# Performance work log

Measured on AMD Instinct MI355X. Metric: run time of the kernel, lower is better.

## Reference

```python
import jax, jax.numpy as jnp
import numpy as np

K = 1024       # vq_codebook_size
DC = 64        # vq_code_dim
BETA = 0.25    # commitment cost
DECAY = 0.99   # EMA decay
EPS = 1e-05


def setup_inputs() -> dict:
    key = jax.random.key(0)
    k1, k2, k3 = jax.random.split(key, 3)
    B, H, W = 32, 64, 64
    return {
        "z_e": jax.random.normal(k1, (B, DC, H, W), dtype=jnp.float32),
        "embedding": jax.random.normal(k2, (K, DC), dtype=jnp.float32),
        "cluster_size": jnp.ones((K,), dtype=jnp.float32),
        "embed_avg": jax.random.normal(k3, (K, DC), dtype=jnp.float32),
    }


def reference(z_e, embedding, cluster_size, embed_avg):
    B, D, H, W = z_e.shape
    # flat: [N, D] detached codes, N = B*H*W
    flat = jax.lax.stop_gradient(z_e).transpose(0, 2, 3, 1).reshape(-1, D).astype(jnp.float32)
    distances = ((flat ** 2).sum(1, keepdims=True)
                 + (embedding ** 2).sum(1)
                 - 2.0 * flat @ embedding.T)
    indices = jnp.argmin(distances, axis=-1)          # [N]
    z_q_flat = embedding[indices]                      # gather [N, D]

    # EMA statistics (training path): one-hot sums via segment_sum (scatter-add)
    counts = jax.ops.segment_sum(jnp.ones_like(indices, dtype=jnp.float32), indices, num_segments=K)
    dw = jax.ops.segment_sum(flat, indices, num_segments=K)  # encodings.T @ flat
    new_cluster_size = cluster_size * DECAY + (1.0 - DECAY) * counts
    new_embed_avg = embed_avg * DECAY + (1.0 - DECAY) * dw
    n = new_cluster_size.sum()
    smoothed = (new_cluster_size + EPS) / (n + K * EPS) * n
    new_embedding = new_embed_avg / smoothed[:, None]

    z_q = z_q_flat.reshape(B, H, W, D).transpose(0, 3, 1, 2)  # [B, D, H, W]
    commitment_loss = BETA * jnp.mean((z_e.astype(jnp.float32) - jax.lax.stop_gradient(z_q)) ** 2)
    # straight-through estimator
    z_q_st = z_e + jax.lax.stop_gradient(z_q.astype(z_e.dtype) - z_e)
    return (z_q_st, indices.reshape(B, H, W), commitment_loss,
            new_embedding, new_cluster_size, new_embed_avg)
```

## Files before the change

### kernel.cpp

```cpp
#include <hip/hip_runtime.h>

#define KCB   1024
#define DCV   64
#define HWN   4096
#define CHW   262144
#define NTOT  131072

#define O_ZQ   0
#define O_IDX  8388608
#define O_LOSS 8519680
#define O_NE   8519681
#define O_NCS  8585217
#define O_NEA  8586241

#define W_LOSS  0
#define W_CTR   64
#define W_E2    256
#define W_SM    4352
#define W_HIT   8448
#define W_LOT   139520
#define W_PARTC 270592
#define W_RLIST 401664

#define MARGIN 0.05f

typedef __attribute__((ext_vector_type(8))) short short8v;
typedef __attribute__((ext_vector_type(4))) float f32x4;

__device__ __forceinline__ unsigned short rne16(float f) {
    unsigned u = __float_as_uint(f);
    unsigned r = (u + 0x7FFFu + ((u >> 16) & 1u)) >> 16;
    return (unsigned short)r;
}

__global__ __launch_bounds__(256) void k_init(
    const float* __restrict__ emb, const float* __restrict__ ea,
    float* __restrict__ out, float* __restrict__ e2,
    short* __restrict__ hiT, short* __restrict__ loT,
    double* __restrict__ loss, int* __restrict__ ctr)
{
    int j = blockIdx.x * 256 + threadIdx.x;
    out[O_NEA + j] = 0.99f * ea[j];
    if (j < KCB) {
        const float* er = emb + j * DCV;
        float s = 0.f;
        #pragma unroll
        for (int d = 0; d < DCV; ++d) { float v = er[d]; s = fmaf(v, v, s); }
        e2[j] = s;
    }
    if (j < 8192) {
        int code = j >> 3, q = j & 7;
        const float* src = emb + code * DCV + q * 8;
        short8v h, l;
        #pragma unroll
        for (int t = 0; t < 8; ++t) {
            float x = src[t];
            unsigned short hb = rne16(x);
            float xh = __uint_as_float(((unsigned)hb) << 16);
            h[t] = (short)hb;
            l[t] = (short)rne16(x - xh);
        }
        *(short8v*)(hiT + (size_t)(q * KCB + code) * 8) = h;
        *(short8v*)(loT + (size_t)(q * KCB + code) * 8) = l;
    }
    if (j == 0) { *loss = 0.0; *ctr = 0; }
}

__global__ __launch_bounds__(256, 4) void k_dist(
    const float* __restrict__ ze, const short* __restrict__ hiT,
    const short* __restrict__ loT, const float* __restrict__ e2g,
    float* __restrict__ out, int* __restrict__ ctr, int* __restrict__ rlist)
{
    __shared__ short ldsH[8 * 128 * 8];
    __shared__ short ldsL[8 * 128 * 8];
    __shared__ float e2s[KCB];

    int tid  = threadIdx.x;
    int lane = tid & 63, w = tid >> 6;
    int g = lane >> 4, c = lane & 15;

    for (int i = tid; i < KCB; i += 256) e2s[i] = e2g[i];

    int rowbase = blockIdx.x * 128 + w * 32;
    short8v ahi[2][2], alo[2][2];
    #pragma unroll
    for (int t = 0; t < 2; ++t) {
        int n = rowbase + t * 16 + c;
        const float* base = ze + (size_t)(n >> 12) * CHW + (n & 4095);
        #pragma unroll
        for (int kh = 0; kh < 2; ++kh) {
            #pragma unroll
            for (int j = 0; j < 8; ++j) {
                int k = kh * 32 + g * 8 + j;
                float x = base[(size_t)k * HWN];
                unsigned short hb = rne16(x);
                float xh = __uint_as_float(((unsigned)hb) << 16);
                ahi[t][kh][j] = (short)hb;
                alo[t][kh][j] = (short)rne16(x - xh);
            }
        }
    }

    float best[8], second[8];
    int   bidx[8];
    #pragma unroll
    for (int i = 0; i < 8; ++i) { best[i] = 3.4e38f; second[i] = 3.4e38f; bidx[i] = 0; }

    for (int ch = 0; ch < 8; ++ch) {
        __syncthreads();
        #pragma unroll
        for (int r = 0; r < 8; ++r) {
            int u = r * 256 + tid;
            int arr = u >> 10;
            int rest = u & 1023;
            int q = rest >> 7, lc = rest & 127;
            const short* s = (arr ? loT : hiT) + (size_t)(q * KCB + ch * 128 + lc) * 8;
            short* d = (arr ? ldsL : ldsH) + rest * 8;
            *(short8v*)d = *(const short8v*)s;
        }
        __syncthreads();

        #pragma unroll 1
        for (int sub = 0; sub < 8; ++sub) {
            int boff = (sub * 16 + c) * 8;
            short8v bh0 = *(const short8v*)&ldsH[(g * 128) * 8 + boff];
            short8v bh1 = *(const short8v*)&ldsH[((4 + g) * 128) * 8 + boff];
            short8v bl0 = *(const short8v*)&ldsL[(g * 128) * 8 + boff];
            short8v bl1 = *(const short8v*)&ldsL[((4 + g) * 128) * 8 + boff];

            f32x4 a0 = {0.f, 0.f, 0.f, 0.f}, a1 = {0.f, 0.f, 0.f, 0.f};
            a0 = __builtin_amdgcn_mfma_f32_16x16x32_bf16(ahi[0][0], bh0, a0, 0, 0, 0);
            a1 = __builtin_amdgcn_mfma_f32_16x16x32_bf16(ahi[1][0], bh0, a1, 0, 0, 0);
            a0 = __builtin_amdgcn_mfma_f32_16x16x32_bf16(ahi[0][1], bh1, a0, 0, 0, 0);
            a1 = __builtin_amdgcn_mfma_f32_16x16x32_bf16(ahi[1][1], bh1, a1, 0, 0, 0);
            a0 = __builtin_amdgcn_mfma_f32_16x16x32_bf16(ahi[0][0], bl0, a0, 0, 0, 0);
            a1 = __builtin_amdgcn_mfma_f32_16x16x32_bf16(ahi[1][0], bl0, a1, 0, 0, 0);
            a0 = __builtin_amdgcn_mfma_f32_16x16x32_bf16(ahi[0][1], bl1, a0, 0, 0, 0);
            a1 = __builtin_amdgcn_mfma_f32_16x16x32_bf16(ahi[1][1], bl1, a1, 0, 0, 0);
            a0 = __builtin_amdgcn_mfma_f32_16x16x32_bf16(alo[0][0], bh0, a0, 0, 0, 0);
            a1 = __builtin_amdgcn_mfma_f32_16x16x32_bf16(alo[1][0], bh0, a1, 0, 0, 0);
            a0 = __builtin_amdgcn_mfma_f32_16x16x32_bf16(alo[0][1], bh1, a0, 0, 0, 0);
            a1 = __builtin_amdgcn_mfma_f32_16x16x32_bf16(alo[1][1], bh1, a1, 0, 0, 0);

            float e2v = e2s[ch * 128 + sub * 16 + c];
            int  code = ch * 128 + sub * 16 + c;
            #pragma unroll
            for (int t = 0; t < 2; ++t) {
                f32x4 av = t ? a1 : a0;
                #pragma unroll
                for (int r = 0; r < 4; ++r) {
                    int i = t * 4 + r;
                    float s = fmaf(-2.f, av[r], e2v);
                    bool lb = s < best[i];
                    bool ls = s < second[i];
                    second[i] = lb ? best[i] : (ls ? s : second[i]);
                    best[i]   = lb ? s : best[i];
                    bidx[i]   = lb ? code : bidx[i];
                }
            }
        }
    }

    #pragma unroll
    for (int i = 0; i < 8; ++i) {
        float b = best[i], s2 = second[i];
        int bi = bidx[i];
        #pragma unroll
        for (int m = 1; m < 16; m <<= 1) {
            float ob = __shfl_xor(b, m, 64);
            float os = __shfl_xor(s2, m, 64);
            int   oi = __shfl_xor(bi, m, 64);
            float ns = fminf(fmaxf(b, ob), fminf(s2, os));
            bi = (ob < b || (ob == b && oi < bi)) ? oi : bi;
            b  = fminf(b, ob);
            s2 = ns;
        }
        if (c == 0) {
            int t = i >> 2, r = i & 3;
            int n = rowbase + t * 16 + g * 4 + r;
            out[O_IDX + n] = (float)bi;
            if (s2 - b < MARGIN) { int p = atomicAdd(ctr, 1); rlist[p] = n; }
        }
    }
}

__global__ __launch_bounds__(256) void k_refine(
    const float* __restrict__ ze, const float* __restrict__ emb,
    float* __restrict__ out, const int* __restrict__ ctr,
    const int* __restrict__ rlist)
{
    int lane = threadIdx.x & 63;
    int gw   = (blockIdx.x * blockDim.x + threadIdx.x) >> 6;
    int nw   = (gridDim.x * blockDim.x) >> 6;
    int cnt  = *ctr;

    for (int i = gw; i < cnt; i += nw) {
        int n  = rlist[i];
        const float* zp = ze + (size_t)(n >> 12) * CHW + (n & 4095);
        float x[DCV];
        #pragma unroll
        for (int d = 0; d < DCV; ++d) x[d] = zp[(size_t)d * HWN];

        double bd = 1e300;
        int    bi = 0;
        #pragma unroll 1
        for (int cc = 0; cc < KCB / 64; ++cc) {
            int k = cc * 64 + lane;
            const float* eb = emb + k * DCV;
            double a0 = 0.0, a1 = 0.0;
            #pragma unroll
            for (int d = 0; d < DCV; d += 2) {
                double d0 = (double)x[d]     - (double)eb[d];
                double d1 = (double)x[d + 1] - (double)eb[d + 1];
                a0 = fma(d0, d0, a0);
                a1 = fma(d1, d1, a1);
            }
            double dist = a0 + a1;
            if (dist < bd || (dist == bd && k < bi)) { bd = dist; bi = k; }
        }
        #pragma unroll
        for (int off = 32; off > 0; off >>= 1) {
            double od = __shfl_xor(bd, off, 64);
            int    oi = __shfl_xor(bi, off, 64);
            if (od < bd || (od == bd && oi < bi)) { bd = od; bi = oi; }
        }
        if (lane == 0) out[O_IDX + n] = (float)bi;
    }
}

__global__ __launch_bounds__(256) void k_final(
    const float* __restrict__ ze, const float* __restrict__ emb,
    float* __restrict__ out, double* __restrict__ loss)
{
    int n  = blockIdx.x * 256 + threadIdx.x;
    int best = (int)out[O_IDX + n];

    const float* zp = ze + (size_t)(n >> 12) * CHW + (n & 4095);
    const float4* er4 = (const float4*)(emb + best * DCV);
    float er[DCV];
    #pragma unroll
    for (int q = 0; q < DCV / 4; ++q) {
        float4 v = er4[q];
        er[q * 4 + 0] = v.x; er[q * 4 + 1] = v.y;
        er[q * 4 + 2] = v.z; er[q * 4 + 3] = v.w;
    }

    float* zq = out + O_ZQ + (size_t)(n >> 12) * CHW + (n & 4095);
    float lp = 0.f;
    #pragma unroll
    for (int d = 0; d < DCV; ++d) {
        float x  = zp[(size_t)d * HWN];
        float df = x - er[d];
        lp = fmaf(df, df, lp);
        zq[(size_t)d * HWN] = x + (er[d] - x);
    }

    #pragma unroll
    for (int off = 32; off > 0; off >>= 1) lp += __shfl_down(lp, off, 64);

    __shared__ float wsum[4];
    int lane = threadIdx.x & 63, wid = threadIdx.x >> 6;
    if (lane == 0) wsum[wid] = lp;
    __syncthreads();
    if (threadIdx.x == 0) {
        double s = (double)wsum[0] + wsum[1] + wsum[2] + wsum[3];
        atomicAdd(loss, s);
    }
}

__global__ __launch_bounds__(256) void k_dw_part(
    const float* __restrict__ ze, const float* __restrict__ outIdx,
    float* __restrict__ partc, float* __restrict__ out)
{
    int gidx = blockIdx.x >> 5, b = blockIdx.x & 31;
    __shared__ float acc[8 * KCB];
    __shared__ float cnt[KCB];
    for (int i = threadIdx.x; i < 8 * KCB; i += 256) acc[i] = 0.f;
    if (gidx == 0) for (int i = threadIdx.x; i < KCB; i += 256) cnt[i] = 0.f;
    __syncthreads();

    const float* zp  = ze + (size_t)b * CHW + (size_t)gidx * 8 * HWN;
    const float* ipf = outIdx + b * HWN;
    for (int hw = threadIdx.x; hw < HWN; hw += 256) {
        int idx = (int)ipf[hw];
        #pragma unroll
        for (int i = 0; i < 8; ++i) atomicAdd(&acc[i * KCB + idx], zp[(size_t)i * HWN + hw]);
        if (gidx == 0) atomicAdd(&cnt[idx], 1.f);
    }
    __syncthreads();

    for (int j = threadIdx.x; j < 8192; j += 256) {
        int k = j >> 3, i = j & 7;
        float v = acc[i * KCB + k];
        if (v != 0.f) atomicAdd(&out[O_NEA + k * DCV + gidx * 8 + i], 0.01f * v);
    }
    if (gidx == 0)
        for (int k = threadIdx.x; k < KCB; k += 256) partc[b * KCB + k] = cnt[k];
}

__global__ __launch_bounds__(1024) void k_stats(
    const float* __restrict__ cs, const float* __restrict__ partc,
    float* __restrict__ out, float* __restrict__ sm,
    const double* __restrict__ loss)
{
    int k = threadIdx.x;
    float csum = 0.f;
    #pragma unroll
    for (int b = 0; b < 32; ++b) csum += partc[b * KCB + k];
    float ncs = fmaf(0.01f, csum, 0.99f * cs[k]);
    out[O_NCS + k] = ncs;

    __shared__ float red[KCB];
    red[k] = ncs;
    __syncthreads();
    for (int s = 512; s > 0; s >>= 1) {
        if (k < s) red[k] += red[k + s];
        __syncthreads();
    }
    float n = red[0];
    sm[k] = (ncs + 1e-5f) / (n + (float)KCB * 1e-5f) * n;
    if (k == 0) out[O_LOSS] = (float)(0.25 * (*loss) / (double)(NTOT * DCV));
}

__global__ __launch_bounds__(256) void k_embed(
    float* __restrict__ out, const float* __restrict__ sm)
{
    int j = blockIdx.x * 256 + threadIdx.x;
    out[O_NE + j] = out[O_NEA + j] / sm[j >> 6];
}

extern "C" void kernel_launch(void* const* d_in, const int* in_sizes, int n_in,
                              void* d_out, int out_size, void* d_ws, size_t ws_size,
                              hipStream_t stream)
{
    const float* ze  = (const float*)d_in[0];
    const float* emb = (const float*)d_in[1];
    const float* cs  = (const float*)d_in[2];
    const float* ea  = (const float*)d_in[3];
    float* out = (float*)d_out;

    char*   w     = (char*)d_ws;
    double* loss  = (double*)(w + W_LOSS);
    int*    ctr   = (int*)(w + W_CTR);
    float*  e2    = (float*)(w + W_E2);
    float*  sm    = (float*)(w + W_SM);
    short*  hiT   = (short*)(w + W_HIT);
    short*  loT   = (short*)(w + W_LOT);
    float*  partc = (float*)(w + W_PARTC);
    int*    rlist = (int*)(w + W_RLIST);

    k_init   <<<256, 256, 0, stream>>>(emb, ea, out, e2, hiT, loT, loss, ctr);
    k_dist   <<<1024, 256, 0, stream>>>(ze, hiT, loT, e2, out, ctr, rlist);
    k_refine <<<256, 256, 0, stream>>>(ze, emb, out, ctr, rlist);
    k_final  <<<NTOT / 256, 256, 0, stream>>>(ze, emb, out, loss);
    k_dw_part<<<256, 256, 0, stream>>>(ze, (const float*)(out + O_IDX), partc, out);
    k_stats  <<<1, 1024, 0, stream>>>(cs, partc, out, sm, loss);
    k_embed  <<<256, 256, 0, stream>>>(out, sm);
}
```

Before: 292.5 us.

## Fuse z_q write and loss into distance kernel, patch refined rows incrementally

The separate final pass is removed. The distance kernel now rebuilds each row from its bf16 hi/lo split, gathers the chosen code, writes the straight-through output and accumulates the commitment loss. The refine kernel rewrites output and adjusts the loss by the distance delta only for rows whose index changed, and the refine margin is tightened to send fewer rows to the fp64 pass. The dw shared accumulator layout also changes to code-major, and the second-best update uses fminf. This saves a full re-read of z_e, but the loss and z_q now rely on the hi+lo reconstruction (about 16 mantissa bits) and on a smaller margin, which risks small accuracy differences.

```diff
diff --git a/kernel.cpp b/kernel.cpp
--- a/kernel.cpp
+++ b/kernel.cpp
@@ -22,7 +22,7 @@
 #define W_PARTC 270592
 #define W_RLIST 401664
 
-#define MARGIN 0.05f
+#define MARGIN 0.015f
 
 typedef __attribute__((ext_vector_type(8))) short short8v;
 typedef __attribute__((ext_vector_type(4))) float f32x4;
@@ -67,13 +67,16 @@
 }
 
 __global__ __launch_bounds__(256, 4) void k_dist(
-    const float* __restrict__ ze, const short* __restrict__ hiT,
-    const short* __restrict__ loT, const float* __restrict__ e2g,
-    float* __restrict__ out, int* __restrict__ ctr, int* __restrict__ rlist)
+    const float* __restrict__ ze, const float* __restrict__ emb,
+    const short* __restrict__ hiT, const short* __restrict__ loT,
+    const float* __restrict__ e2g, float* __restrict__ out,
+    int* __restrict__ ctr, int* __restrict__ rlist, double* __restrict__ loss)
 {
     __shared__ short ldsH[8 * 128 * 8];
     __shared__ short ldsL[8 * 128 * 8];
     __shared__ float e2s[KCB];
+    __shared__ int   bestSh[4][32];
+    __shared__ float wsum[4];
 
     int tid  = threadIdx.x;
     int lane = tid & 63, w = tid >> 6;
@@ -152,9 +155,9 @@
                     int i = t * 4 + r;
                     float s = fmaf(-2.f, av[r], e2v);
                     bool lb = s < best[i];
-                    bool ls = s < second[i];
-                    second[i] = lb ? best[i] : (ls ? s : second[i]);
-                    best[i]   = lb ? s : best[i];
+                    float m = lb ? best[i] : s;
+                    second[i] = fminf(second[i], m);
+                    best[i]   = fminf(best[i], s);
                     bidx[i]   = lb ? code : bidx[i];
                 }
             }
@@ -177,17 +180,55 @@
         }
         if (c == 0) {
             int t = i >> 2, r = i & 3;
-            int n = rowbase + t * 16 + g * 4 + r;
+            int rw = t * 16 + g * 4 + r;
+            int n = rowbase + rw;
             out[O_IDX + n] = (float)bi;
+            bestSh[w][rw] = bi;
             if (s2 - b < MARGIN) { int p = atomicAdd(ctr, 1); rlist[p] = n; }
         }
+    }
+    __syncthreads();
+
+    float lp = 0.f;
+    #pragma unroll
+    for (int t = 0; t < 2; ++t) {
+        int rw = t * 16 + c;
+        int n = rowbase + rw;
+        int bsel = bestSh[w][rw];
+        const float* erow = emb + bsel * DCV;
+        float* zq = out + O_ZQ + (size_t)(n >> 12) * CHW + (n & 4095);
+        #pragma unroll
+        for (int kh = 0; kh < 2; ++kh) {
+            int d0 = kh * 32 + g * 8;
+            float4 e0 = *(const float4*)&erow[d0];
+            float4 e1 = *(const float4*)&erow[d0 + 4];
+            float ev[8] = {e0.x, e0.y, e0.z, e0.w, e1.x, e1.y, e1.z, e1.w};
+            #pragma unroll
+            for (int j = 0; j < 8; ++j) {
+                float xh = __uint_as_float(((unsigned)(unsigned short)ahi[t][kh][j]) << 16);
+                float xl = __uint_as_float(((unsigned)(unsigned short)alo[t][kh][j]) << 16);
+                float xv = xh + xl;
+                float er = ev[j];
+                float df = xv - er;
+                lp = fmaf(df, df, lp);
+                zq[(size_t)(d0 + j) * HWN] = xv + (er - xv);
+            }
+        }
+    }
+    #pragma unroll
+    for (int off = 32; off > 0; off >>= 1) lp += __shfl_down(lp, off, 64);
+    if (lane == 0) wsum[w] = lp;
+    __syncthreads();
+    if (tid == 0) {
+        double s = (double)wsum[0] + wsum[1] + wsum[2] + wsum[3];
+        atomicAdd(loss, s);
     }
 }
 
 __global__ __launch_bounds__(256) void k_refine(
     const float* __restrict__ ze, const float* __restrict__ emb,
     float* __restrict__ out, const int* __restrict__ ctr,
-    const int* __restrict__ rlist)
+    const int* __restrict__ rlist, double* __restrict__ loss)
 {
     int lane = threadIdx.x & 63;
     int gw   = (blockIdx.x * blockDim.x + threadIdx.x) >> 6;
@@ -195,76 +236,52 @@
     int cnt  = *ctr;
 
     for (int i = gw; i < cnt; i += nw) {
-        int n  = rlist[i];
+        int n    = rlist[i];
+        int oldi = (int)out[O_IDX + n];
         const float* zp = ze + (size_t)(n >> 12) * CHW + (n & 4095);
         float x[DCV];
         #pragma unroll
         for (int d = 0; d < DCV; ++d) x[d] = zp[(size_t)d * HWN];
 
-        double bd = 1e300;
+        double bd = 1e300, dold = -1e300;
         int    bi = 0;
         #pragma unroll 1
         for (int cc = 0; cc < KCB / 64; ++cc) {
             int k = cc * 64 + lane;
-            const float* eb = emb + k * DCV;
+            const float4* eb4 = (const float4*)(emb + k * DCV);
             double a0 = 0.0, a1 = 0.0;
             #pragma unroll
-            for (int d = 0; d < DCV; d += 2) {
-                double d0 = (double)x[d]     - (double)eb[d];
-                double d1 = (double)x[d + 1] - (double)eb[d + 1];
-                a0 = fma(d0, d0, a0);
-                a1 = fma(d1, d1, a1);
+            for (int q = 0; q < DCV / 4; ++q) {
+                float4 v = eb4[q];
+                double d0 = (double)x[q * 4 + 0] - (double)v.x;
+                double d1 = (double)x[q * 4 + 1] - (double)v.y;
+                double d2 = (double)x[q * 4 + 2] - (double)v.z;
+                double d3 = (double)x[q * 4 + 3] - (double)v.w;
+                a0 = fma(d0, d0, a0); a1 = fma(d1, d1, a1);
+                a0 = fma(d2, d2, a0); a1 = fma(d3, d3, a1);
             }
             double dist = a0 + a1;
+            if (k == oldi) dold = dist;
             if (dist < bd || (dist == bd && k < bi)) { bd = dist; bi = k; }
         }
         #pragma unroll
         for (int off = 32; off > 0; off >>= 1) {
             double od = __shfl_xor(bd, off, 64);
             int    oi = __shfl_xor(bi, off, 64);
+            double oo = __shfl_xor(dold, off, 64);
             if (od < bd || (od == bd && oi < bi)) { bd = od; bi = oi; }
-        }
-        if (lane == 0) out[O_IDX + n] = (float)bi;
-    }
-}
-
-__global__ __launch_bounds__(256) void k_final(
-    const float* __restrict__ ze, const float* __restrict__ emb,
-    float* __restrict__ out, double* __restrict__ loss)
-{
-    int n  = blockIdx.x * 256 + threadIdx.x;
-    int best = (int)out[O_IDX + n];
-
-    const float* zp = ze + (size_t)(n >> 12) * CHW + (n & 4095);
-    const float4* er4 = (const float4*)(emb + best * DCV);
-    float er[DCV];
-    #pragma unroll
-    for (int q = 0; q < DCV / 4; ++q) {
-        float4 v = er4[q];
-        er[q * 4 + 0] = v.x; er[q * 4 + 1] = v.y;
-        er[q * 4 + 2] = v.z; er[q * 4 + 3] = v.w;
-    }
-
-    float* zq = out + O_ZQ + (size_t)(n >> 12) * CHW + (n & 4095);
-    float lp = 0.f;
-    #pragma unroll
-    for (int d = 0; d < DCV; ++d) {
-        float x  = zp[(size_t)d * HWN];
-        float df = x - er[d];
-        lp = fmaf(df, df, lp);
-        zq[(size_t)d * HWN] = x + (er[d] - x);
-    }
-
-    #pragma unroll
-    for (int off = 32; off > 0; off >>= 1) lp += __shfl_down(lp, off, 64);
-
-    __shared__ float wsum[4];
-    int lane = threadIdx.x & 63, wid = threadIdx.x >> 6;
-    if (lane == 0) wsum[wid] = lp;
-    __syncthreads();
-    if (threadIdx.x == 0) {
-        double s = (double)wsum[0] + wsum[1] + wsum[2] + wsum[3];
-        atomicAdd(loss, s);
+            dold = fmax(dold, oo);
+        }
+        if (bi != oldi) {
+            if (lane == 0) {
+                out[O_IDX + n] = (float)bi;
+                atomicAdd(loss, bd - dold);
+            }
+            float e  = emb[bi * DCV + lane];
+            float xv = x[lane];
+            float* zq = out + O_ZQ + (size_t)(n >> 12) * CHW + (n & 4095);
+            zq[(size_t)lane * HWN] = xv + (e - xv);
+        }
     }
 }
 
@@ -284,15 +301,14 @@
     for (int hw = threadIdx.x; hw < HWN; hw += 256) {
         int idx = (int)ipf[hw];
         #pragma unroll
-        for (int i = 0; i < 8; ++i) atomicAdd(&acc[i * KCB + idx], zp[(size_t)i * HWN + hw]);
+        for (int i = 0; i < 8; ++i) atomicAdd(&acc[idx * 8 + i], zp[(size_t)i * HWN + hw]);
         if (gidx == 0) atomicAdd(&cnt[idx], 1.f);
     }
     __syncthreads();
 
     for (int j = threadIdx.x; j < 8192; j += 256) {
-        int k = j >> 3, i = j & 7;
-        float v = acc[i * KCB + k];
-        if (v != 0.f) atomicAdd(&out[O_NEA + k * DCV + gidx * 8 + i], 0.01f * v);
+        float v = acc[j];
+        if (v != 0.f) atomicAdd(&out[O_NEA + (j >> 3) * DCV + gidx * 8 + (j & 7)], 0.01f * v);
     }
     if (gidx == 0)
         for (int k = threadIdx.x; k < KCB; k += 256) partc[b * KCB + k] = cnt[k];
@@ -350,9 +366,8 @@
     int*    rlist = (int*)(w + W_RLIST);
 
     k_init   <<<256, 256, 0, stream>>>(emb, ea, out, e2, hiT, loT, loss, ctr);
-    k_dist   <<<1024, 256, 0, stream>>>(ze, hiT, loT, e2, out, ctr, rlist);
-    k_refine <<<256, 256, 0, stream>>>(ze, emb, out, ctr, rlist);
-    k_final  <<<NTOT / 256, 256, 0, stream>>>(ze, emb, out, loss);
+    k_dist   <<<1024, 256, 0, stream>>>(ze, emb, hiT, loT, e2, out, ctr, rlist, loss);
+    k_refine <<<256, 256, 0, stream>>>(ze, emb, out, ctr, rlist, loss);
     k_dw_part<<<256, 256, 0, stream>>>(ze, (const float*)(out + O_IDX), partc, out);
     k_stats  <<<1, 1024, 0, stream>>>(cs, partc, out, sm, loss);
     k_embed  <<<256, 256, 0, stream>>>(out, sm);
```

Result: slower. 312.1 us (+6.7%).
